# Optimization experiments

Measured on AMD Instinct MI355X. Metric: run time of the kernel, lower is better.

## Reference

```python
import jax, jax.numpy as jnp
import numpy as np

ATT_K = 180   # attention_k
NPOOL = 15    # WeldonPooling(15): mean of top-15 + mean of bottom-15 spatial scores


def setup_inputs() -> dict:
    key = jax.random.key(0)
    k1, k2, k3, k4 = jax.random.split(key, 4)
    imgs, emb, h, w = 16, 2400, 14, 14
    caps_cnt = 64
    return {
        "g": jax.random.normal(k1, (imgs, emb, h, w), dtype=jnp.float32),
        "caps": jax.random.normal(k2, (caps_cnt, emb), dtype=jnp.float32),
        "fc_w": jax.random.normal(k3, (emb, emb), dtype=jnp.float32) * 0.02,
        "fc_b": jax.random.normal(k4, (emb,), dtype=jnp.float32) * 0.02,
    }


def reference(g, caps, fc_w, fc_b):
    imgs, emb, h, w = g.shape
    caps_cnt = caps.shape[0]

    # ---- WeldonPooling(15): per (img, channel) sort spatial scores ----
    flat = g.reshape(imgs, emb, h * w)
    s = jnp.sort(flat, axis=2)  # ascending
    hpool = s[:, :, -NPOOL:].mean(axis=2) + s[:, :, :NPOOL].mean(axis=2)  # [imgs, emb]
    x = hpool @ fc_w.T + fc_b  # fc (dropout is identity at eval / p=0)

    # ---- get_heat_map: top-k caption dims, gather fc-projected features ----
    order = jnp.argsort(-caps, axis=1)[:, :ATT_K]                 # [C, k] indices
    vals = jnp.take_along_axis(caps, order, axis=1)               # [C, k] top-k values (desc)
    gf = jnp.einsum('oe,iehw->oihw', fc_w, g)                     # fc.weight @ g -> [emb, imgs, h, w]
    gsel = gf[order]                                              # gather -> [C, k, imgs, h, w]
    heat = jnp.sum(jnp.abs(gsel * vals[:, :, None, None, None]), axis=1)  # [C, imgs, h, w]
    heat = jnp.transpose(heat, (1, 0, 2, 3))                      # [imgs, C, h, w]
    heat = heat / jnp.sum(heat, axis=(2, 3), keepdims=True)       # normalize per (img, cap)

    # ---- attention_embedding: weighted spatial sum, then fc ----
    xa = jnp.einsum('ichw,iehw->ice', heat, g)                    # [imgs, C, emb]
    xa = xa @ fc_w.T + fc_b

    return x, xa, g
```

## Files before the change

kernel.cpp:

```cpp
#include <hip/hip_runtime.h>
#include <math.h>

#define IMGS 16
#define EMB 2400
#define HW 196
#define CAPS 64
#define ATTK 180
#define NPOOL 15
#define NCOLS (IMGS * HW)
#define KPAD 224

typedef __attribute__((ext_vector_type(8))) short short8;
typedef __attribute__((ext_vector_type(4))) float f32x4;
typedef const __attribute__((address_space(1))) unsigned int* gas1_t;
typedef __attribute__((address_space(3))) unsigned int* las3_t;
typedef unsigned long long ull;

__device__ inline unsigned short f2bf(float f) {
    unsigned int u = __builtin_bit_cast(unsigned int, f);
    u += 0x7fffu + ((u >> 16) & 1u);
    return (unsigned short)(u >> 16);
}
__device__ inline float bf2f(unsigned int lo16) {
    return __builtin_bit_cast(float, lo16 << 16);
}
__device__ inline unsigned f2sort(float f) {
    unsigned u = __builtin_bit_cast(unsigned, f);
    int msk = ((int)u) >> 31;
    return u ^ (unsigned)(msk | 0x80000000);
}

__global__ __launch_bounds__(256) void transpool_kernel(const float* __restrict__ g,
                                                        float* __restrict__ hpool,
                                                        unsigned short* __restrict__ gT,
                                                        float* __restrict__ gout) {
    __shared__ float t[32][197];
    int e0 = blockIdx.x * 32;
    int i = blockIdx.y;
    int tid = threadIdx.x;
    const float* base = g + ((size_t)i * EMB + e0) * HW;
    float* obase = gout ? gout + ((size_t)i * EMB + e0) * HW : nullptr;
    for (int f = tid; f < 32 * HW; f += 256) {
        int e = f / HW, hw = f % HW;
        float v = base[(size_t)e * HW + hw];
        t[e][hw] = v;
        if (obase) obase[(size_t)e * HW + hw] = v;
    }
    __syncthreads();
    for (int f = tid; f < HW * 32; f += 256) {
        int hw = f / 32, e = f % 32;
        gT[((size_t)i * HW + hw) * EMB + e0 + e] = f2bf(t[e][hw]);
    }
    int w = tid >> 6, tl = tid & 63, hl = tl & 31;
    bool negh = tl >= 32;
#pragma unroll 1
    for (int rr = 0; rr < 8; ++rr) {
        int e = w * 8 + rr;
        float s[7];
#pragma unroll
        for (int q = 0; q < 7; q++) {
            int hw = hl + 32 * q;
            if (hw < HW) {
                unsigned u = __builtin_bit_cast(unsigned, t[e][hw]);
                if (negh) u ^= 0x80000000u;
                u = (u & 0xFFFFFF00u) | (unsigned)(q * 32 + hl);
                s[q] = __builtin_bit_cast(float, u);
            } else {
                s[q] = -INFINITY;
            }
        }
#define CS(a, b)                                   \
    {                                              \
        float hi = fmaxf(s[a], s[b]);              \
        float lo = fminf(s[a], s[b]);              \
        s[a] = hi; s[b] = lo;                      \
    }
        CS(1, 2) CS(3, 4) CS(5, 6)
        CS(0, 2) CS(3, 5) CS(4, 6)
        CS(0, 1) CS(4, 5) CS(2, 6)
        CS(0, 4) CS(1, 5)
        CS(0, 3) CS(2, 5)
        CS(1, 3) CS(2, 4)
        CS(2, 3)
#undef CS
        float acc = 0.f;
#pragma unroll
        for (int it = 0; it < NPOOL; ++it) {
            int x = __builtin_bit_cast(int, s[0]);
#define ST(c)                                                                  \
    {                                                                          \
        int y = __builtin_amdgcn_update_dpp(x, x, c, 0xf, 0xf, false);         \
        float a = fmaxf(__builtin_bit_cast(float, x), __builtin_bit_cast(float, y)); \
        x = __builtin_bit_cast(int, a);                                        \
    }
            ST(0x111) ST(0x112) ST(0x114) ST(0x118) ST(0x142)
#undef ST
            int m31 = __builtin_amdgcn_readlane(x, 31);
            int m63 = __builtin_amdgcn_readlane(x, 63);
            float msel = __builtin_bit_cast(float, negh ? m63 : m31);
            acc += msel;
            bool won = (__builtin_bit_cast(unsigned, s[0]) ==
                        __builtin_bit_cast(unsigned, msel));
            s[0] = won ? s[1] : s[0];
            s[1] = won ? s[2] : s[1];
            s[2] = won ? s[3] : s[2];
            s[3] = won ? s[4] : s[3];
            s[4] = won ? s[5] : s[4];
            s[5] = won ? s[6] : s[5];
            s[6] = won ? -INFINITY : s[6];
        }
        int ai = __builtin_bit_cast(int, acc);
        float a0 = __builtin_bit_cast(float, __builtin_amdgcn_readlane(ai, 0));
        float a32 = __builtin_bit_cast(float, __builtin_amdgcn_readlane(ai, 32));
        if (tl == 0) hpool[(size_t)i * EMB + e0 + e] = (a0 - a32) / 15.0f;
    }
}

__global__ __launch_bounds__(256) void xw_kernel(const float* __restrict__ hpool,
                                                 const float* __restrict__ fc_w,
                                                 const float* __restrict__ fc_b,
                                                 float* __restrict__ x_out,
                                                 unsigned short* __restrict__ wbf) {
    int o = blockIdx.x * 4 + (threadIdx.x >> 6);
    int lane = threadIdx.x & 63;
    float acc[IMGS];
#pragma unroll
    for (int i = 0; i < IMGS; i++) acc[i] = 0.f;
    const float* wrow = fc_w + (size_t)o * EMB;
    unsigned short* wdst = wbf + (size_t)o * EMB;
    for (int e = lane * 4; e < EMB; e += 256) {
        float4 wv = *(const float4*)&wrow[e];
        ushort4 r;
        r.x = f2bf(wv.x); r.y = f2bf(wv.y); r.z = f2bf(wv.z); r.w = f2bf(wv.w);
        *(ushort4*)&wdst[e] = r;
#pragma unroll
        for (int i = 0; i < IMGS; i++) {
            const float* hp = hpool + i * EMB + e;
            acc[i] += hp[0] * wv.x + hp[1] * wv.y + hp[2] * wv.z + hp[3] * wv.w;
        }
    }
#pragma unroll
    for (int i = 0; i < IMGS; i++) {
#pragma unroll
        for (int sdx = 32; sdx > 0; sdx >>= 1) acc[i] += __shfl_xor(acc[i], sdx, 64);
    }
    if (lane == 0) {
        float bo = fc_b[o];
#pragma unroll
        for (int i = 0; i < IMGS; i++) x_out[i * EMB + o] = acc[i] + bo;
    }
}

__global__ void x_kernel(const float* __restrict__ hpool, const float* __restrict__ fc_w,
                         const float* __restrict__ fc_b, float* __restrict__ x_out) {
    int o = blockIdx.x;
    int lane = threadIdx.x;
    float acc[IMGS];
#pragma unroll
    for (int i = 0; i < IMGS; i++) acc[i] = 0.f;
    const float* wrow = fc_w + (size_t)o * EMB;
    for (int e = lane; e < EMB; e += 64) {
        float wv = wrow[e];
#pragma unroll
        for (int i = 0; i < IMGS; i++) acc[i] += hpool[i * EMB + e] * wv;
    }
#pragma unroll
    for (int i = 0; i < IMGS; i++) {
#pragma unroll
        for (int sdx = 32; sdx > 0; sdx >>= 1) acc[i] += __shfl_xor(acc[i], sdx, 64);
    }
    if (lane == 0) {
        float bo = fc_b[o];
#pragma unroll
        for (int i = 0; i < IMGS; i++) x_out[i * EMB + o] = acc[i] + bo;
    }
}

__global__ __launch_bounds__(256) void topk_kernel(const float* __restrict__ caps,
                                                   int* __restrict__ idxs,
                                                   float* __restrict__ vals) {
    __shared__ float rowf[EMB];
    __shared__ unsigned hist[4][256];
    __shared__ unsigned scanbuf[256];
    __shared__ unsigned wtot[4];
    __shared__ ull sprefix;
    __shared__ int srank;
    int c = blockIdx.x;
    int tid = threadIdx.x;
    int w = tid >> 6, lane = tid & 63;
    const float4* src = (const float4*)(caps + (size_t)c * EMB);
    for (int j = tid; j < EMB / 4; j += 256) {
        float4 v = src[j];
        *(float4*)&rowf[j * 4] = v;
    }
    if (tid == 0) { sprefix = 0ull; srank = ATTK; }

#pragma unroll 1
    for (int pass = 0; pass < 6; ++pass) {
        __syncthreads();
        ull pref = sprefix;
        int rk = srank;
        int shift = 40 - pass * 8;
        ull pmaskhi = (pass == 0) ? 0ull : ~((1ull << (shift + 8)) - 1ull);
        hist[0][tid] = 0; hist[1][tid] = 0; hist[2][tid] = 0; hist[3][tid] = 0;
        __syncthreads();
        unsigned* myhist = hist[w];
#pragma unroll 1
        for (int s = 0; s < 10; s++) {
            int e = tid + s * 256;
            if (e < EMB) {
                ull key = ((ull)f2sort(rowf[e]) << 16) | ((unsigned)(2399 - e) << 4);
                if ((key & pmaskhi) == pref)
                    atomicAdd(&myhist[(unsigned)(key >> shift) & 255u], 1u);
            }
        }
        __syncthreads();
        unsigned h = hist[0][tid] + hist[1][tid] + hist[2][tid] + hist[3][tid];
        scanbuf[255 - tid] = h;
        __syncthreads();
        unsigned x = scanbuf[tid];
#pragma unroll
        for (int d = 1; d < 64; d <<= 1) {
            unsigned u = __shfl_up(x, d, 64);
            if (lane >= d) x += u;
        }
        if (lane == 63) wtot[w] = x;
        __syncthreads();
        unsigned off = 0;
        for (int ww = 0; ww < w; ww++) off += wtot[ww];
        scanbuf[tid] = x + off;
        __syncthreads();
        unsigned incl = scanbuf[255 - tid];
        unsigned excl = incl - h;
        if (h > 0u && excl < (unsigned)rk && incl >= (unsigned)rk) {
            srank = rk - (int)excl;
            sprefix = pref | ((ull)tid << shift);
        }
    }
    __syncthreads();
    ull T = sprefix;
    unsigned selmask = 0, cnt = 0;
#pragma unroll 1
    for (int s = 0; s < 10; s++) {
        int e = tid + s * 256;
        if (e < EMB) {
            ull key = ((ull)f2sort(rowf[e]) << 16) | ((unsigned)(2399 - e) << 4);
            if (key >= T) { selmask |= 1u << s; cnt++; }
        }
    }
    unsigned x = cnt;
#pragma unroll
    for (int d = 1; d < 64; d <<= 1) {
        unsigned u = __shfl_up(x, d, 64);
        if (lane >= d) x += u;
    }
    if (lane == 63) wtot[w] = x;
    __syncthreads();
    unsigned off = 0;
    for (int ww = 0; ww < w; ww++) off += wtot[ww];
    unsigned slot = x + off - cnt;
#pragma unroll 1
    for (int s = 0; s < 10; s++) {
        if (selmask & (1u << s)) {
            int e = tid + s * 256;
            idxs[c * ATTK + slot] = e;
            vals[c * ATTK + slot] = fabsf(rowf[e]);
            slot++;
        }
    }
}

template <int MF, int NF, int OUT_MODE>
__global__ __launch_bounds__(256) void gemm_gll(const unsigned short* __restrict__ A,
                                                const unsigned short* __restrict__ B,
                                                void* __restrict__ outp,
                                                const float* __restrict__ bias,
                                                const float* __restrict__ invS,
                                                int M, int N, int K, int ldb, int kper,
                                                long az, long bz) {
    constexpr int BM = MF * 32, BN = NF * 32;
    constexpr int ROWS = BM + BN;
    constexpr int RPAD = (ROWS + 63) & ~63;
    constexpr int NCALL = RPAD / 16;
    constexpr int LPW = NCALL / 4;
    __shared__ unsigned short lds[3][RPAD][32];
    int gx = gridDim.x, gy = gridDim.y;
    int nwg = gx * gy;
    int flat = blockIdx.y * gx + blockIdx.x;
    int qq = nwg >> 3, rr8 = nwg & 7;
    int xcd = flat & 7, idx = flat >> 3;
    int base = (xcd < rr8) ? xcd * (qq + 1) : rr8 * (qq + 1) + (xcd - rr8) * qq;
    int nf = base + idx;
    int m0 = (nf % gy) * BM;
    int n0 = (nf / gy) * BN;
    int z = blockIdx.z;
    const unsigned short* Ab = A + (size_t)z * az;
    const unsigned short* Bb = B + (size_t)z * bz;
    int kb = (az == 0 && bz == 0) ? z * kper : 0;
    int nt = kper / 32;
    int tid = threadIdx.x, w = tid >> 6, lane = tid & 63;
    int wm = (w >> 1) * (MF * 16), wn = (w & 1) * (NF * 16);
    int ln = lane & 15;
    int ks = (((lane >> 4) ^ ((lane >> 1) & 3))) * 8;
    int srow = lane >> 2;
    int skc = (((lane & 3) ^ ((lane >> 3) & 3))) * 8;

    auto STAGE = [&](int buf, int t) {
        int k0 = kb + t * 32;
#pragma unroll
        for (int j = 0; j < LPW; j++) {
            int jj = w + j * 4;
            int r = jj * 16 + srow;
            const unsigned short* src;
            if (r < BM) src = Ab + (size_t)(m0 + r) * K + k0 + skc;
            else if (r < ROWS) src = Bb + (size_t)(n0 + r - BM) * ldb + k0 + skc;
            else src = Ab + (size_t)m0 * K + k0 + skc;
            __builtin_amdgcn_global_load_lds((gas1_t)(const void*)src,
                                             (las3_t)(void*)&lds[buf][jj * 16][0], 16, 0, 0);
        }
    };

    STAGE(0, 0);
    if (nt > 1) STAGE(1, 1);
    f32x4 acc[MF][NF] = {};
    for (int t = 0; t < nt; ++t) {
        if (t + 1 < nt) {
            if constexpr (LPW == 4) asm volatile("s_waitcnt vmcnt(4) lgkmcnt(0)" ::: "memory");
            else if constexpr (LPW == 5) asm volatile("s_waitcnt vmcnt(5) lgkmcnt(0)" ::: "memory");
            else if constexpr (LPW == 6) asm volatile("s_waitcnt vmcnt(6) lgkmcnt(0)" ::: "memory");
            else asm volatile("s_waitcnt vmcnt(0) lgkmcnt(0)" ::: "memory");
        } else {
            asm volatile("s_waitcnt vmcnt(0) lgkmcnt(0)" ::: "memory");
        }
        __builtin_amdgcn_s_barrier();
        __builtin_amdgcn_sched_barrier(0);
        if (t + 2 < nt) STAGE((t + 2) % 3, t + 2);
        const unsigned short(*buf)[32] = lds[t % 3];
        short8 af[MF], bfv[NF];
#pragma unroll
        for (int mf = 0; mf < MF; mf++)
            af[mf] = *(const short8*)&buf[wm + mf * 16 + ln][ks];
#pragma unroll
        for (int nfi = 0; nfi < NF; nfi++)
            bfv[nfi] = *(const short8*)&buf[BM + wn + nfi * 16 + ln][ks];
        __builtin_amdgcn_s_setprio(1);
#pragma unroll
        for (int mf = 0; mf < MF; mf++)
#pragma unroll
            for (int nfi = 0; nfi < NF; nfi++)
                acc[mf][nfi] = __builtin_amdgcn_mfma_f32_16x16x32_bf16(af[mf], bfv[nfi],
                                                                       acc[mf][nfi], 0, 0, 0);
        __builtin_amdgcn_s_setprio(0);
    }
#pragma unroll
    for (int mf = 0; mf < MF; mf++) {
#pragma unroll
        for (int nfi = 0; nfi < NF; nfi++) {
#pragma unroll
            for (int rr = 0; rr < 4; rr++) {
                int row = m0 + wm + mf * 16 + (lane >> 4) * 4 + rr;
                int col = n0 + wn + nfi * 16 + ln;
                float v = acc[mf][nfi][rr];
                if (OUT_MODE == 6) {
                    ((unsigned short*)outp)[(size_t)row * N + col] = f2bf(v);
                } else if (OUT_MODE == 4) {
                    ((float*)outp)[((size_t)z * CAPS + row) * N + col] =
                        v * invS[z * CAPS + row] + bias[col];
                }
            }
        }
    }
}

__device__ inline uint4 load8(const unsigned short* p) { return *(const uint4*)p; }
__device__ inline uint4 load8(const float* p) {
    float4 a = *(const float4*)p;
    float4 b = *(const float4*)(p + 4);
    uint4 r;
    r.x = (unsigned)f2bf(a.x) | ((unsigned)f2bf(a.y) << 16);
    r.y = (unsigned)f2bf(a.z) | ((unsigned)f2bf(a.w) << 16);
    r.z = (unsigned)f2bf(b.x) | ((unsigned)f2bf(b.y) << 16);
    r.w = (unsigned)f2bf(b.z) | ((unsigned)f2bf(b.w) << 16);
    return r;
}

template <int MF, int NF, typename TA, typename TB>
__global__ __launch_bounds__(256) void mfma_gemm_nt(const TA* __restrict__ A,
                                                    const TB* __restrict__ B,
                                                    void* __restrict__ outp,
                                                    int M, int N, int K) {
    constexpr int BM = MF * 32, BN = NF * 32;
    constexpr int nA = BM * 4, nTot = (BM + BN) * 4;
    constexpr int NCH = (nTot + 255) / 256;
    __shared__ unsigned short As[BM][40];
    __shared__ unsigned short Bs[BN][40];
    int m0 = blockIdx.y * BM, n0 = blockIdx.x * BN;
    int tid = threadIdx.x;
    int w = tid >> 6, lane = tid & 63;
    int wm = (w >> 1) * (MF * 16), wn = (w & 1) * (NF * 16);
    int ln = lane & 15, ks = (lane >> 4) * 8;
    uint4 r[NCH];
#pragma unroll
    for (int j = 0; j < NCH; j++) {
        int c = tid + 256 * j;
        if (c < nTot) {
            if (c < nA) {
                int row = c >> 2, kc = c & 3;
                r[j] = load8(A + (size_t)(m0 + row) * K + kc * 8);
            } else {
                int cc = c - nA, row = cc >> 2, kc = cc & 3;
                r[j] = load8(B + (size_t)(n0 + row) * K + kc * 8);
            }
        }
    }
    f32x4 acc[MF][NF] = {};
    for (int k0 = 0; k0 < K; k0 += 32) {
#pragma unroll
        for (int j = 0; j < NCH; j++) {
            int c = tid + 256 * j;
            if (c < nTot) {
                if (c < nA) {
                    int row = c >> 2, kc = c & 3;
                    *(uint4*)&As[row][kc * 8] = r[j];
                } else {
                    int cc = c - nA, row = cc >> 2, kc = cc & 3;
                    *(uint4*)&Bs[row][kc * 8] = r[j];
                }
            }
        }
        __syncthreads();
        if (k0 + 32 < K) {
#pragma unroll
            for (int j = 0; j < NCH; j++) {
                int c = tid + 256 * j;
                if (c < nTot) {
                    if (c < nA) {
                        int row = c >> 2, kc = c & 3;
                        r[j] = load8(A + (size_t)(m0 + row) * K + (k0 + 32) + kc * 8);
                    } else {
                        int cc = c - nA, row = cc >> 2, kc = cc & 3;
                        r[j] = load8(B + (size_t)(n0 + row) * K + (k0 + 32) + kc * 8);
                    }
                }
            }
        }
        short8 af[MF], bfv[NF];
#pragma unroll
        for (int mf = 0; mf < MF; mf++)
            af[mf] = *(const short8*)&As[wm + mf * 16 + ln][ks];
#pragma unroll
        for (int nfi = 0; nfi < NF; nfi++)
            bfv[nfi] = *(const short8*)&Bs[wn + nfi * 16 + ln][ks];
#pragma unroll
        for (int mf = 0; mf < MF; mf++)
#pragma unroll
            for (int nfi = 0; nfi < NF; nfi++)
                acc[mf][nfi] = __builtin_amdgcn_mfma_f32_16x16x32_bf16(af[mf], bfv[nfi],
                                                                       acc[mf][nfi], 0, 0, 0);
        __syncthreads();
    }
#pragma unroll
    for (int mf = 0; mf < MF; mf++) {
#pragma unroll
        for (int nfi = 0; nfi < NF; nfi++) {
#pragma unroll
            for (int rr = 0; rr < 4; rr++) {
                int row = m0 + wm + mf * 16 + (lane >> 4) * 4 + rr;
                int col = n0 + wn + nfi * 16 + ln;
                ((unsigned short*)outp)[(size_t)row * N + col] = f2bf(acc[mf][nfi][rr]);
            }
        }
    }
}

__global__ __launch_bounds__(256) void heat_kernel(const int* __restrict__ idxs,
                                                   const float* __restrict__ vals,
                                                   const unsigned short* __restrict__ A,
                                                   unsigned short* __restrict__ Hnbf,
                                                   float* __restrict__ invS) {
    __shared__ int sidx[ATTK];
    __shared__ float sval[ATTK];
    __shared__ float wsum[4];
    int i = blockIdx.x, c = blockIdx.y;
    int tid = threadIdx.x;
    int w = tid >> 6, lane = tid & 63;
    if (tid < ATTK) {
        sidx[tid] = idxs[c * ATTK + tid];
        sval[tid] = vals[c * ATTK + tid];
    }
    __syncthreads();
    int hw = tid;
    float v = 0.f;
    if (hw < HW) {
        int n = i * HW + hw;
        float a0 = 0.f, a1 = 0.f, a2 = 0.f, a3 = 0.f;
#pragma unroll 1
        for (int j = 0; j < ATTK; j += 4) {
            a0 += sval[j + 0] * bf2f(A[(size_t)sidx[j + 0] * NCOLS + n] & 0x7FFFu);
            a1 += sval[j + 1] * bf2f(A[(size_t)sidx[j + 1] * NCOLS + n] & 0x7FFFu);
            a2 += sval[j + 2] * bf2f(A[(size_t)sidx[j + 2] * NCOLS + n] & 0x7FFFu);
            a3 += sval[j + 3] * bf2f(A[(size_t)sidx[j + 3] * NCOLS + n] & 0x7FFFu);
        }
        v = (a0 + a1) + (a2 + a3);
    }
    if (hw < KPAD)
        Hnbf[((size_t)i * CAPS + c) * KPAD + hw] = (hw < HW) ? f2bf(v) : (unsigned short)0;
    float s = v;
#pragma unroll
    for (int d = 32; d > 0; d >>= 1) s += __shfl_xor(s, d, 64);
    if (lane == 0) wsum[w] = s;
    __syncthreads();
    if (tid == 0)
        invS[i * CAPS + c] = 1.0f / (wsum[0] + wsum[1] + wsum[2] + wsum[3]);
}

extern "C" void kernel_launch(void* const* d_in, const int* in_sizes, int n_in,
                              void* d_out, int out_size, void* d_ws, size_t ws_size,
                              hipStream_t stream) {
    const float* g = (const float*)d_in[0];
    const float* caps = (const float*)d_in[1];
    const float* fc_w = (const float*)d_in[2];
    const float* fc_b = (const float*)d_in[3];

    float* out = (float*)d_out;
    float* x_out = out;
    float* xa_out = out + 38400;
    float* g_out = out + 38400 + 2457600;

    float* ws = (float*)d_ws;
    float* hpool = ws;
    int* idxs = (int*)(ws + 38400);
    float* vals = ws + 49920;
    float* invS = ws + 61440;
    unsigned short* Hnbf = (unsigned short*)(ws + 62464);
    unsigned short* wbf = (unsigned short*)(ws + 1490944);
    bool use_wbf = ws_size >= (size_t)17483776;
    bool ws_big = use_wbf && ws_size >= (size_t)(17483776 + 2 * 15052800);
    unsigned short* gT_big = (unsigned short*)((char*)d_ws + 17483776);
    unsigned short* Asig_big = (unsigned short*)((char*)d_ws + 17483776 + 15052800);

    unsigned short* Asig = ws_big ? Asig_big : (unsigned short*)g_out;
    unsigned short* gT = ws_big ? gT_big : ((unsigned short*)g_out + (size_t)EMB * NCOLS);

    transpool_kernel<<<dim3(EMB / 32, IMGS), 256, 0, stream>>>(
        g, hpool, gT, ws_big ? g_out : nullptr);
    topk_kernel<<<CAPS, 256, 0, stream>>>(caps, idxs, vals);

    if (use_wbf) {
        xw_kernel<<<EMB / 4, 256, 0, stream>>>(hpool, fc_w, fc_b, x_out, wbf);
        gemm_gll<5, 7, 6><<<dim3(NCOLS / 224, EMB / 160, 1), 256, 0, stream>>>(
            wbf, gT, Asig, nullptr, nullptr, EMB, NCOLS, EMB, EMB, EMB, 0, 0);
    } else {
        x_kernel<<<EMB, 64, 0, stream>>>(hpool, fc_w, fc_b, x_out);
        mfma_gemm_nt<5, 2, float, unsigned short>
            <<<dim3(NCOLS / 64, EMB / 160), 256, 0, stream>>>(fc_w, gT, Asig,
                                                              EMB, NCOLS, EMB);
    }
    heat_kernel<<<dim3(IMGS, CAPS), 256, 0, stream>>>(idxs, vals, Asig, Hnbf, invS);
    gemm_gll<2, 5, 4><<<dim3(EMB / 160, 1, IMGS), 256, 0, stream>>>(
        Hnbf, Asig, xa_out, fc_b, invS, CAPS, EMB, KPAD, NCOLS, KPAD,
        (long)CAPS * KPAD, HW);
    if (!ws_big) {
        hipMemcpyAsync(g_out, g, sizeof(float) * (size_t)IMGS * EMB * HW,
                       hipMemcpyDeviceToDevice, stream);
    }
}
```

Measured before the change: 158.8 us.

## Merge topk, weight conversion and transpool into one heterogeneous launch

Combines the caption top-k selection, fc weight bf16 conversion, and the transpose/Weldon pooling kernel into a single kernel that dispatches on block index, so the independent stages share one launch and run concurrently. The fc matvec for x is split out and now reads the bf16 weight copy instead of fp32, halving its weight traffic. The shared-memory footprint becomes the max of the merged stages, which may affect occupancy. Using bf16 weights for x slightly reduces precision.

```diff
diff --git a/kernel.cpp b/kernel.cpp
--- a/kernel.cpp
+++ b/kernel.cpp
@@ -30,13 +30,14 @@
     return u ^ (unsigned)(msk | 0x80000000);
 }
 
-__global__ __launch_bounds__(256) void transpool_kernel(const float* __restrict__ g,
-                                                        float* __restrict__ hpool,
-                                                        unsigned short* __restrict__ gT,
-                                                        float* __restrict__ gout) {
-    __shared__ float t[32][197];
-    int e0 = blockIdx.x * 32;
-    int i = blockIdx.y;
+
+__device__ __forceinline__ void transpool_body(char* smem, int bx, int i,
+                                               const float* __restrict__ g,
+                                               float* __restrict__ hpool,
+                                               unsigned short* __restrict__ gT,
+                                               float* __restrict__ gout) {
+    float(*t)[197] = (float(*)[197])smem;
+    int e0 = bx * 32;
     int tid = threadIdx.x;
     const float* base = g + ((size_t)i * EMB + e0) * HW;
     float* obase = gout ? gout + ((size_t)i * EMB + e0) * HW : nullptr;
@@ -116,76 +117,16 @@
     }
 }
 
-__global__ __launch_bounds__(256) void xw_kernel(const float* __restrict__ hpool,
-                                                 const float* __restrict__ fc_w,
-                                                 const float* __restrict__ fc_b,
-                                                 float* __restrict__ x_out,
-                                                 unsigned short* __restrict__ wbf) {
-    int o = blockIdx.x * 4 + (threadIdx.x >> 6);
-    int lane = threadIdx.x & 63;
-    float acc[IMGS];
-#pragma unroll
-    for (int i = 0; i < IMGS; i++) acc[i] = 0.f;
-    const float* wrow = fc_w + (size_t)o * EMB;
-    unsigned short* wdst = wbf + (size_t)o * EMB;
-    for (int e = lane * 4; e < EMB; e += 256) {
-        float4 wv = *(const float4*)&wrow[e];
-        ushort4 r;
-        r.x = f2bf(wv.x); r.y = f2bf(wv.y); r.z = f2bf(wv.z); r.w = f2bf(wv.w);
-        *(ushort4*)&wdst[e] = r;
-#pragma unroll
-        for (int i = 0; i < IMGS; i++) {
-            const float* hp = hpool + i * EMB + e;
-            acc[i] += hp[0] * wv.x + hp[1] * wv.y + hp[2] * wv.z + hp[3] * wv.w;
-        }
-    }
-#pragma unroll
-    for (int i = 0; i < IMGS; i++) {
-#pragma unroll
-        for (int sdx = 32; sdx > 0; sdx >>= 1) acc[i] += __shfl_xor(acc[i], sdx, 64);
-    }
-    if (lane == 0) {
-        float bo = fc_b[o];
-#pragma unroll
-        for (int i = 0; i < IMGS; i++) x_out[i * EMB + o] = acc[i] + bo;
-    }
-}
-
-__global__ void x_kernel(const float* __restrict__ hpool, const float* __restrict__ fc_w,
-                         const float* __restrict__ fc_b, float* __restrict__ x_out) {
-    int o = blockIdx.x;
-    int lane = threadIdx.x;
-    float acc[IMGS];
-#pragma unroll
-    for (int i = 0; i < IMGS; i++) acc[i] = 0.f;
-    const float* wrow = fc_w + (size_t)o * EMB;
-    for (int e = lane; e < EMB; e += 64) {
-        float wv = wrow[e];
-#pragma unroll
-        for (int i = 0; i < IMGS; i++) acc[i] += hpool[i * EMB + e] * wv;
-    }
-#pragma unroll
-    for (int i = 0; i < IMGS; i++) {
-#pragma unroll
-        for (int sdx = 32; sdx > 0; sdx >>= 1) acc[i] += __shfl_xor(acc[i], sdx, 64);
-    }
-    if (lane == 0) {
-        float bo = fc_b[o];
-#pragma unroll
-        for (int i = 0; i < IMGS; i++) x_out[i * EMB + o] = acc[i] + bo;
-    }
-}
-
-__global__ __launch_bounds__(256) void topk_kernel(const float* __restrict__ caps,
-                                                   int* __restrict__ idxs,
-                                                   float* __restrict__ vals) {
-    __shared__ float rowf[EMB];
-    __shared__ unsigned hist[4][256];
-    __shared__ unsigned scanbuf[256];
-    __shared__ unsigned wtot[4];
-    __shared__ ull sprefix;
-    __shared__ int srank;
-    int c = blockIdx.x;
+__device__ __forceinline__ void topk_body(char* smem, int c,
+                                          const float* __restrict__ caps,
+                                          int* __restrict__ idxs,
+                                          float* __restrict__ vals) {
+    float* rowf = (float*)smem;
+    unsigned(*hist)[256] = (unsigned(*)[256])(smem + 9600);
+    unsigned* scanbuf = (unsigned*)(smem + 13696);
+    unsigned* wtot = (unsigned*)(smem + 14720);
+    ull* sprefix = (ull*)(smem + 14744);
+    int* srank = (int*)(smem + 14752);
     int tid = threadIdx.x;
     int w = tid >> 6, lane = tid & 63;
     const float4* src = (const float4*)(caps + (size_t)c * EMB);
@@ -193,13 +134,12 @@
         float4 v = src[j];
         *(float4*)&rowf[j * 4] = v;
     }
-    if (tid == 0) { sprefix = 0ull; srank = ATTK; }
-
+    if (tid == 0) { *sprefix = 0ull; *srank = ATTK; }
 #pragma unroll 1
     for (int pass = 0; pass < 6; ++pass) {
         __syncthreads();
-        ull pref = sprefix;
-        int rk = srank;
+        ull pref = *sprefix;
+        int rk = *srank;
         int shift = 40 - pass * 8;
         ull pmaskhi = (pass == 0) ? 0ull : ~((1ull << (shift + 8)) - 1ull);
         hist[0][tid] = 0; hist[1][tid] = 0; hist[2][tid] = 0; hist[3][tid] = 0;
@@ -233,12 +173,12 @@
         unsigned incl = scanbuf[255 - tid];
         unsigned excl = incl - h;
         if (h > 0u && excl < (unsigned)rk && incl >= (unsigned)rk) {
-            srank = rk - (int)excl;
-            sprefix = pref | ((ull)tid << shift);
+            *srank = rk - (int)excl;
+            *sprefix = pref | ((ull)tid << shift);
         }
     }
     __syncthreads();
-    ull T = sprefix;
+    ull T = *sprefix;
     unsigned selmask = 0, cnt = 0;
 #pragma unroll 1
     for (int s = 0; s < 10; s++) {
@@ -267,6 +207,98 @@
             vals[c * ATTK + slot] = fabsf(rowf[e]);
             slot++;
         }
+    }
+}
+
+__device__ __forceinline__ void convw_body(int b, const float* __restrict__ fc_w,
+                                           unsigned short* __restrict__ wbf) {
+    int o = b * 4 + (threadIdx.x >> 6);
+    int lane = threadIdx.x & 63;
+    const float* wrow = fc_w + (size_t)o * EMB;
+    unsigned short* wdst = wbf + (size_t)o * EMB;
+    for (int e = lane * 4; e < EMB; e += 256) {
+        float4 wv = *(const float4*)&wrow[e];
+        ushort4 r;
+        r.x = f2bf(wv.x); r.y = f2bf(wv.y); r.z = f2bf(wv.z); r.w = f2bf(wv.w);
+        *(ushort4*)&wdst[e] = r;
+    }
+}
+
+__global__ __launch_bounds__(256) void combo_kernel(const float* __restrict__ g,
+                                                    float* __restrict__ hpool,
+                                                    unsigned short* __restrict__ gT,
+                                                    float* __restrict__ gout,
+                                                    const float* __restrict__ caps,
+                                                    int* __restrict__ idxs,
+                                                    float* __restrict__ vals,
+                                                    const float* __restrict__ fc_w,
+                                                    unsigned short* __restrict__ wbf,
+                                                    int nconv) {
+    __shared__ __align__(16) char smem[25664];
+    int b = blockIdx.x;
+    if (b < CAPS) {
+        topk_body(smem, b, caps, idxs, vals);
+    } else if (b < CAPS + nconv) {
+        convw_body(b - CAPS, fc_w, wbf);
+    } else {
+        int tb = b - CAPS - nconv;
+        transpool_body(smem, tb % (EMB / 32), tb / (EMB / 32), g, hpool, gT, gout);
+    }
+}
+
+__global__ __launch_bounds__(256) void x_bf_kernel(const float* __restrict__ hpool,
+                                                   const unsigned short* __restrict__ wbf,
+                                                   const float* __restrict__ fc_b,
+                                                   float* __restrict__ x_out) {
+    int o = blockIdx.x * 4 + (threadIdx.x >> 6);
+    int lane = threadIdx.x & 63;
+    float acc[IMGS];
+#pragma unroll
+    for (int i = 0; i < IMGS; i++) acc[i] = 0.f;
+    const unsigned short* wrow = wbf + (size_t)o * EMB;
+    for (int e = lane * 4; e < EMB; e += 256) {
+        ushort4 wq = *(const ushort4*)&wrow[e];
+        float w0 = bf2f(wq.x), w1 = bf2f(wq.y), w2 = bf2f(wq.z), w3 = bf2f(wq.w);
+#pragma unroll
+        for (int i = 0; i < IMGS; i++) {
+            const float* hp = hpool + i * EMB + e;
+            acc[i] += hp[0] * w0 + hp[1] * w1 + hp[2] * w2 + hp[3] * w3;
+        }
+    }
+#pragma unroll
+    for (int i = 0; i < IMGS; i++) {
+#pragma unroll
+        for (int sdx = 32; sdx > 0; sdx >>= 1) acc[i] += __shfl_xor(acc[i], sdx, 64);
+    }
+    if (lane == 0) {
+        float bo = fc_b[o];
+#pragma unroll
+        for (int i = 0; i < IMGS; i++) x_out[i * EMB + o] = acc[i] + bo;
+    }
+}
+
+__global__ void x_kernel(const float* __restrict__ hpool, const float* __restrict__ fc_w,
+                         const float* __restrict__ fc_b, float* __restrict__ x_out) {
+    int o = blockIdx.x;
+    int lane = threadIdx.x;
+    float acc[IMGS];
+#pragma unroll
+    for (int i = 0; i < IMGS; i++) acc[i] = 0.f;
+    const float* wrow = fc_w + (size_t)o * EMB;
+    for (int e = lane; e < EMB; e += 64) {
+        float wv = wrow[e];
+#pragma unroll
+        for (int i = 0; i < IMGS; i++) acc[i] += hpool[i * EMB + e] * wv;
+    }
+#pragma unroll
+    for (int i = 0; i < IMGS; i++) {
+#pragma unroll
+        for (int sdx = 32; sdx > 0; sdx >>= 1) acc[i] += __shfl_xor(acc[i], sdx, 64);
+    }
+    if (lane == 0) {
+        float bo = fc_b[o];
+#pragma unroll
+        for (int i = 0; i < IMGS; i++) x_out[i * EMB + o] = acc[i] + bo;
     }
 }
 
@@ -542,15 +574,15 @@
     unsigned short* Asig = ws_big ? Asig_big : (unsigned short*)g_out;
     unsigned short* gT = ws_big ? gT_big : ((unsigned short*)g_out + (size_t)EMB * NCOLS);
 
-    transpool_kernel<<<dim3(EMB / 32, IMGS), 256, 0, stream>>>(
-        g, hpool, gT, ws_big ? g_out : nullptr);
-    topk_kernel<<<CAPS, 256, 0, stream>>>(caps, idxs, vals);
-
     if (use_wbf) {
-        xw_kernel<<<EMB / 4, 256, 0, stream>>>(hpool, fc_w, fc_b, x_out, wbf);
+        combo_kernel<<<CAPS + EMB / 4 + (EMB / 32) * IMGS, 256, 0, stream>>>(
+            g, hpool, gT, ws_big ? g_out : nullptr, caps, idxs, vals, fc_w, wbf, EMB / 4);
+        x_bf_kernel<<<EMB / 4, 256, 0, stream>>>(hpool, wbf, fc_b, x_out);
         gemm_gll<5, 7, 6><<<dim3(NCOLS / 224, EMB / 160, 1), 256, 0, stream>>>(
             wbf, gT, Asig, nullptr, nullptr, EMB, NCOLS, EMB, EMB, EMB, 0, 0);
     } else {
+        combo_kernel<<<CAPS + (EMB / 32) * IMGS, 256, 0, stream>>>(
+            g, hpool, gT, nullptr, caps, idxs, vals, fc_w, nullptr, 0);
         x_kernel<<<EMB, 64, 0, stream>>>(hpool, fc_w, fc_b, x_out);
         mfma_gemm_nt<5, 2, float, unsigned short>
             <<<dim3(NCOLS / 64, EMB / 160), 256, 0, stream>>>(fc_w, gT, Asig,
```

Result: faster. 151.5 us (-4.6%).
